# Kernel tuning notes

Measured on AMD Instinct MI355X. Metric: run time of the kernel, lower is better.

The kernel has to match this reference:

```python
import jax, jax.numpy as jnp
import numpy as np

NEUTRAL = -jnp.inf  # tropical_max semifield neutral element


def _tropical_max_conv(imgs, kernel, stride, padding, dilation):
    """out[b,o,y,x] = max_{c,i,j} imgs_pad[b,c,y*s+i*d, x*s+j*d] + k_flipped[o,c,i,j].

    Matches BroadcastConv with BroadcastSemifield.tropical_max() (kind='conv',
    so the kernel is flipped along its spatial dims), groups=1,
    group_broadcasting=False. Streams over the kh*kw kernel positions with a
    running max instead of materializing the unfold tensor.
    """
    B, C, H, W = imgs.shape
    O, Ck, kh, kw = kernel.shape
    assert Ck == C
    k = kernel[:, :, ::-1, ::-1]  # flip for kind='conv'
    pad = jnp.pad(
        imgs,
        ((0, 0), (0, 0), (padding, padding), (padding, padding)),
        constant_values=NEUTRAL,
    )
    out_h = (H + 2 * padding - dilation * (kh - 1) - 1) // stride + 1
    out_w = (W + 2 * padding - dilation * (kw - 1) - 1) // stride + 1
    out = jnp.full((B, O, out_h, out_w), NEUTRAL, dtype=imgs.dtype)
    for i in range(kh):  # small fixed kernel loop (25 iters)
        for j in range(kw):
            patch = pad[:, :,
                        i * dilation: i * dilation + (out_h - 1) * stride + 1: stride,
                        j * dilation: j * dilation + (out_w - 1) * stride + 1: stride]
            # [B,1,C,Y,X] + [1,O,C,1,1] -> max over C -> [B,O,Y,X]
            cand = jnp.max(patch[:, None] + k[None, :, :, i, j][:, :, :, None, None],
                           axis=2)
            out = jnp.maximum(out, cand)
    return out


def setup_inputs() -> dict:
    key = jax.random.key(0)
    k1, k2 = jax.random.split(key)
    imgs = jax.random.normal(k1, (4, 32, 128, 128), dtype=jnp.float32)
    kernel = jax.random.normal(k2, (32, 32, 5, 5), dtype=jnp.float32)
    return {"imgs": imgs, "kernel": kernel, "stride": 1, "padding": 2, "dilation": 1}


def reference(imgs, kernel, stride, padding, dilation):
    return _tropical_max_conv(imgs, kernel, stride, padding, dilation)
```

## Files before the change

### kernel.cpp

```cpp
#include <hip/hip_runtime.h>
#include <math.h>


#define TY 8
#define PITCH 132
#define ROWS 12
#define TILE (ROWS * PITCH)
#define NSLOT 7

__global__ __launch_bounds__(256, 2)
void tropical_conv_kernel(const float* __restrict__ img,
                          const float* __restrict__ ker,
                          float* __restrict__ out) {
    const int bid = blockIdx.x;
    const int yb = bid & 15;
    const int ob = (bid >> 4) & 7;
    const int b  = bid >> 7;
    const int y0 = yb * TY;
    const int obase = ob * 4;

    const int tid = threadIdx.x;
    const int tx = tid & 31;
    const int ty = tid >> 5;

    __shared__ __align__(16) float s_img[2][TILE];

    int goff[NSLOT];
    #pragma unroll
    for (int k = 0; k < NSLOT; ++k) {
        int idx = tid + k * 256;
        int row = idx / PITCH;
        int col = idx - row * PITCH;
        int gy = y0 + row - 2;
        int gx = col - 2;
        bool slot = idx < TILE;
        bool ok = slot && ((unsigned)gy < 128u) && ((unsigned)gx < 128u);
        goff[k] = ok ? (gy * 128 + gx) : -1;
        if (slot && !ok) {
            s_img[0][idx] = -INFINITY;
            s_img[1][idx] = -INFINITY;
        }
    }

    const float* imgb = img + (size_t)b * (32 * 128 * 128);

    float acc[4][4];
    #pragma unroll
    for (int o = 0; o < 4; ++o)
        #pragma unroll
        for (int xx = 0; xx < 4; ++xx)
            acc[o][xx] = -INFINITY;

    float rbuf[NSLOT];
    #pragma unroll
    for (int k = 0; k < NSLOT; ++k)
        if (goff[k] >= 0) rbuf[k] = imgb[goff[k]];
    #pragma unroll
    for (int k = 0; k < NSLOT; ++k)
        if (goff[k] >= 0) s_img[0][tid + k * 256] = rbuf[k];
    __syncthreads();

    int p = 0;
    for (int c = 0; c < 32; ++c) {
        if (c < 31) {
            const float* imgc = imgb + ((c + 1) << 14);
            #pragma unroll
            for (int k = 0; k < NSLOT; ++k)
                if (goff[k] >= 0) rbuf[k] = imgc[goff[k]];
        }

        const float* srow = s_img[p];
        #pragma unroll
        for (int i = 0; i < 5; ++i) {
            const float4 r0 = *(const float4*)&srow[(ty + i) * PITCH + tx * 4];
            const float4 r1 = *(const float4*)&srow[(ty + i) * PITCH + tx * 4 + 4];
            const float r[8] = {r0.x, r0.y, r0.z, r0.w, r1.x, r1.y, r1.z, r1.w};

            float w[5][4];
            #pragma unroll
            for (int o = 0; o < 4; ++o) {
                const float* kr = ker + (obase + o) * 800 + c * 25 + (4 - i) * 5;
                #pragma unroll
                for (int j = 0; j < 5; ++j)
                    w[j][o] = kr[4 - j];
            }

            #pragma unroll
            for (int jp = 0; jp < 2; ++jp) {
                #pragma unroll
                for (int o = 0; o < 4; ++o)
                    #pragma unroll
                    for (int xx = 0; xx < 4; ++xx)
                        acc[o][xx] = fmaxf(fmaxf(acc[o][xx],
                                                 r[2 * jp + xx] + w[2 * jp][o]),
                                           r[2 * jp + 1 + xx] + w[2 * jp + 1][o]);
            }
            #pragma unroll
            for (int o = 0; o < 4; ++o)
                #pragma unroll
                for (int xx = 0; xx < 4; ++xx)
                    acc[o][xx] = fmaxf(acc[o][xx], r[4 + xx] + w[4][o]);
        }

        if (c < 31) {
            #pragma unroll
            for (int k = 0; k < NSLOT; ++k)
                if (goff[k] >= 0) s_img[p ^ 1][tid + k * 256] = rbuf[k];
        }
        __syncthreads();
        p ^= 1;
    }

    #pragma unroll
    for (int o = 0; o < 4; ++o) {
        float4 v = make_float4(acc[o][0], acc[o][1], acc[o][2], acc[o][3]);
        *(float4*)&out[((size_t)(b * 32 + obase + o) * 128 + y0 + ty) * 128 + tx * 4] = v;
    }
}

extern "C" void kernel_launch(void* const* d_in, const int* in_sizes, int n_in,
                              void* d_out, int out_size, void* d_ws, size_t ws_size,
                              hipStream_t stream) {
    const float* img = (const float*)d_in[0];
    const float* ker = (const float*)d_in[1];
    float* out = (float*)d_out;
    tropical_conv_kernel<<<512, 256, 0, stream>>>(img, ker, out);
}
```

Measured before the change: 155.0 us.

## Shrink per-thread tile to 2 columns, double blocks, use v_max3 inline asm

```diff
diff --git a/kernel.cpp b/kernel.cpp
--- a/kernel.cpp
+++ b/kernel.cpp
@@ -2,26 +2,33 @@
 #include <math.h>
 
 
-#define TY 8
+#define TY 4
 #define PITCH 132
-#define ROWS 12
+#define ROWS 8
 #define TILE (ROWS * PITCH)
-#define NSLOT 7
+#define NSLOT 5
 
-__global__ __launch_bounds__(256, 2)
+__device__ __forceinline__ float max3f(float a, float b, float c) {
+    float d;
+    asm("v_max3_f32 %0, %1, %2, %3" : "=v"(d) : "v"(a), "v"(b), "v"(c));
+    return d;
+}
+
+__global__ __launch_bounds__(256, 4)
 void tropical_conv_kernel(const float* __restrict__ img,
                           const float* __restrict__ ker,
                           float* __restrict__ out) {
     const int bid = blockIdx.x;
-    const int yb = bid & 15;
-    const int ob = (bid >> 4) & 7;
-    const int b  = bid >> 7;
+    const int yb = bid & 31;
+    const int ob = (bid >> 5) & 7;
+    const int b  = bid >> 8;
     const int y0 = yb * TY;
     const int obase = ob * 4;
 
     const int tid = threadIdx.x;
-    const int tx = tid & 31;
-    const int ty = tid >> 5;
+    const int tx = tid & 63;
+    const int ty = tid >> 6;
+    const int x0 = tx * 2;
 
     __shared__ __align__(16) float s_img[2][TILE];
 
@@ -44,12 +51,12 @@
 
     const float* imgb = img + (size_t)b * (32 * 128 * 128);
 
-    float acc[4][4];
+    float acc[4][2];
     #pragma unroll
-    for (int o = 0; o < 4; ++o)
-        #pragma unroll
-        for (int xx = 0; xx < 4; ++xx)
-            acc[o][xx] = -INFINITY;
+    for (int o = 0; o < 4; ++o) {
+        acc[o][0] = -INFINITY;
+        acc[o][1] = -INFINITY;
+    }
 
     float rbuf[NSLOT];
     #pragma unroll
@@ -72,9 +79,10 @@
         const float* srow = s_img[p];
         #pragma unroll
         for (int i = 0; i < 5; ++i) {
-            const float4 r0 = *(const float4*)&srow[(ty + i) * PITCH + tx * 4];
-            const float4 r1 = *(const float4*)&srow[(ty + i) * PITCH + tx * 4 + 4];
-            const float r[8] = {r0.x, r0.y, r0.z, r0.w, r1.x, r1.y, r1.z, r1.w};
+            const float2 r01 = *(const float2*)&srow[(ty + i) * PITCH + x0];
+            const float2 r23 = *(const float2*)&srow[(ty + i) * PITCH + x0 + 2];
+            const float2 r45 = *(const float2*)&srow[(ty + i) * PITCH + x0 + 4];
+            const float r[6] = {r01.x, r01.y, r23.x, r23.y, r45.x, r45.y};
 
             float w[5][4];
             #pragma unroll
@@ -86,20 +94,17 @@
             }
 
             #pragma unroll
-            for (int jp = 0; jp < 2; ++jp) {
-                #pragma unroll
-                for (int o = 0; o < 4; ++o)
-                    #pragma unroll
-                    for (int xx = 0; xx < 4; ++xx)
-                        acc[o][xx] = fmaxf(fmaxf(acc[o][xx],
-                                                 r[2 * jp + xx] + w[2 * jp][o]),
-                                           r[2 * jp + 1 + xx] + w[2 * jp + 1][o]);
-            }
-            #pragma unroll
             for (int o = 0; o < 4; ++o)
                 #pragma unroll
-                for (int xx = 0; xx < 4; ++xx)
+                for (int xx = 0; xx < 2; ++xx) {
+                    float t0 = r[0 + xx] + w[0][o];
+                    float t1 = r[1 + xx] + w[1][o];
+                    acc[o][xx] = max3f(acc[o][xx], t0, t1);
+                    float t2 = r[2 + xx] + w[2][o];
+                    float t3 = r[3 + xx] + w[3][o];
+                    acc[o][xx] = max3f(acc[o][xx], t2, t3);
                     acc[o][xx] = fmaxf(acc[o][xx], r[4 + xx] + w[4][o]);
+                }
         }
 
         if (c < 31) {
@@ -113,8 +118,8 @@
 
     #pragma unroll
     for (int o = 0; o < 4; ++o) {
-        float4 v = make_float4(acc[o][0], acc[o][1], acc[o][2], acc[o][3]);
-        *(float4*)&out[((size_t)(b * 32 + obase + o) * 128 + y0 + ty) * 128 + tx * 4] = v;
+        float2 v = make_float2(acc[o][0], acc[o][1]);
+        *(float2*)&out[((size_t)(b * 32 + obase + o) * 128 + y0 + ty) * 128 + x0] = v;
     }
 }
 
@@ -124,5 +129,5 @@
     const float* img = (const float*)d_in[0];
     const float* ker = (const float*)d_in[1];
     float* out = (float*)d_out;
-    tropical_conv_kernel<<<512, 256, 0, stream>>>(img, ker, out);
+    tropical_conv_kernel<<<1024, 256, 0, stream>>>(img, ker, out);
 }
```

After: 136.8 us. 1.13x faster.
